# Performance work log

Hardware: AMD Instinct MI355X
Metric: run time of the kernel (lower is better)

The kernel has to match this reference:

```python
import jax, jax.numpy as jnp
import numpy as np

DT = 1.0       # integration timestep
THRESH = 0.5   # firing threshold (standard in this family of SNN repos)


def setup_inputs() -> dict:
    key = jax.random.key(0)
    ks = jax.random.split(key, 6)
    B, Din, Dout = 32768, 256, 512
    input_spike = jax.random.uniform(ks[0], (B, Din), dtype=jnp.float32)
    mem = jnp.zeros((B, Dout), jnp.float32)
    spike = jnp.zeros((B, Dout), jnp.float32)
    s_in = 1.0 / np.sqrt(Din)
    s_h = 1.0 / np.sqrt(Dout)
    W_dense = jax.random.uniform(ks[1], (Dout, Din), minval=-s_in, maxval=s_in, dtype=jnp.float32)
    b_dense = jax.random.uniform(ks[2], (Dout,), minval=-s_in, maxval=s_in, dtype=jnp.float32)
    W_rec = jax.random.uniform(ks[3], (Dout, Dout), minval=-s_h, maxval=s_h, dtype=jnp.float32)
    b_rec = jax.random.uniform(ks[4], (Dout,), minval=-s_h, maxval=s_h, dtype=jnp.float32)
    tau_m = 20.0 + 5.0 * jax.random.normal(ks[5], (Dout,), dtype=jnp.float32)
    return dict(input_spike=input_spike, mem=mem, spike=spike,
                W_dense=W_dense, b_dense=b_dense, W_rec=W_rec, b_rec=b_rec,
                tau_m=tau_m)


def reference(input_spike, mem, spike, W_dense, b_dense, W_rec, b_rec, tau_m):
    # d_input = dense(input_spike) + recurrent(spike)
    d_input = (jnp.einsum('bi,oi->bo', input_spike, W_dense) + b_dense
               + jnp.einsum('bh,oh->bo', spike, W_rec) + b_rec)
    # LIF neuron dynamics: exponential membrane decay, soft reset, heaviside spike
    alpha = jnp.exp(-DT / tau_m)                                   # [Dout]
    mem_new = mem * alpha + (1.0 - alpha) * d_input - THRESH * spike
    spike_new = (mem_new - THRESH > 0).astype(mem_new.dtype)
    return mem_new, spike_new
```

## Files before the change

### kernel.cpp

```cpp
#include <hip/hip_runtime.h>
#include <math.h>

typedef short  short8  __attribute__((ext_vector_type(8)));
typedef short  short4v __attribute__((ext_vector_type(4)));
typedef float  f32x4   __attribute__((ext_vector_type(4)));

#define BATCH 32768
#define DIN   256
#define DOUT  512
#define BM    128
#define BN    64

#define WS_FLAGS 0
#define WS_WD2   4096
#define WS_WR2   (4096 + 262144)
#define WS_X2    (266240 + 524288)

__device__ __forceinline__ short f2bf(float v) {
    unsigned u = __float_as_uint(v);
    u += 0x7fffu + ((u >> 16) & 1u);
    return (short)(u >> 16);
}

__global__ __launch_bounds__(1024) void spike_flag_kernel(
    const float* __restrict__ SPK, int* __restrict__ flags)
{
    __shared__ int s_any;
    if (threadIdx.x == 0) s_any = 0;
    __syncthreads();
    const f32x4* p = (const f32x4*)(SPK + (size_t)blockIdx.x * BM * DOUT);
    unsigned bits = 0;
#pragma unroll
    for (int i = 0; i < 16; i++) {
        f32x4 v = p[threadIdx.x + i * 1024];
        bits |= __float_as_uint(v[0]) | __float_as_uint(v[1])
              | __float_as_uint(v[2]) | __float_as_uint(v[3]);
    }
    if (bits) s_any = 1;
    __syncthreads();
    if (threadIdx.x == 0) flags[blockIdx.x] = s_any;
}

__global__ __launch_bounds__(256) void cvt_bf16_kernel(
    const float* __restrict__ src, short* __restrict__ dst, int n4)
{
    int i = blockIdx.x * 256 + threadIdx.x;
    if (i >= n4) return;
    f32x4 v = ((const f32x4*)src)[i];
    ((short4v*)dst)[i] = (short4v){f2bf(v[0]), f2bf(v[1]), f2bf(v[2]), f2bf(v[3])};
}

__global__ __launch_bounds__(256, 3) void spike_rnn_lif_kernel(
    const short* __restrict__ X2,
    const float* __restrict__ MEM,
    const float* __restrict__ SPK,
    const short* __restrict__ Wd2,
    const float* __restrict__ bd,
    const short* __restrict__ Wr2,
    const float* __restrict__ br,
    const float* __restrict__ tau,
    const int*   __restrict__ flags,
    float* __restrict__ out)
{
    __shared__ float sT[64 * 68];

    const int tid  = threadIdx.x;
    const int lane = tid & 63;
    const int w    = tid >> 6;
    const int wm   = w & 1;
    const int wn   = w >> 1;
    const int bn   = blockIdx.x;
    const int bm   = blockIdx.y;
    const int m0   = bm * BM;
    const int n0   = bn * BN;
    const int col  = lane & 15;
    const int quad = lane >> 4;

    const bool has_spk = (flags[bm] != 0);

    const int c4   = tid & 15;
    const int ncol = n0 + c4 * 4;
    f32x4 mv0[4];
#pragma unroll
    for (int it = 0; it < 4; it++) {
        int row = m0 + ((tid + it * 256) >> 4);
        mv0[it] = __builtin_nontemporal_load(
                      (const f32x4*)(MEM + (size_t)row * DOUT + ncol));
    }

    f32x4 acc[4][2];
#pragma unroll
    for (int i = 0; i < 4; i++)
#pragma unroll
        for (int j = 0; j < 2; j++)
            acc[i][j] = (f32x4){0.f, 0.f, 0.f, 0.f};

    {
        const short* Abase = X2  + (size_t)(m0 + wm * 64 + col) * DIN + quad * 8;
        const short* Bbase = Wd2 + (size_t)(n0 + wn * 32 + col) * DIN + quad * 8;

#define LOAD_AB(kk, aa, bb)                                                   \
        do {                                                                  \
            int k_ = (kk) * 32;                                               \
            _Pragma("unroll")                                                 \
            for (int t = 0; t < 4; t++)                                       \
                aa[t] = *(const short8*)(Abase + (size_t)t * 16 * DIN + k_);  \
            _Pragma("unroll")                                                 \
            for (int t = 0; t < 2; t++)                                       \
                bb[t] = *(const short8*)(Bbase + (size_t)t * 16 * DIN + k_);  \
        } while (0)

#define MFMA_AB(aa, bb)                                                       \
        do {                                                                  \
            _Pragma("unroll")                                                 \
            for (int i = 0; i < 4; i++)                                       \
                _Pragma("unroll")                                             \
                for (int j = 0; j < 2; j++)                                   \
                    acc[i][j] = __builtin_amdgcn_mfma_f32_16x16x32_bf16(      \
                        aa[i], bb[j], acc[i][j], 0, 0, 0);                    \
        } while (0)

        short8 a0[4], b0[2], a1[4], b1[2];
        LOAD_AB(0, a0, b0);
#pragma unroll
        for (int kp = 0; kp < 4; kp++) {
            LOAD_AB(2 * kp + 1, a1, b1);
            MFMA_AB(a0, b0);
            if (kp < 3) LOAD_AB(2 * kp + 2, a0, b0);
            MFMA_AB(a1, b1);
        }
#undef LOAD_AB
    }

    if (has_spk) {
        const float* Abase = SPK + (size_t)(m0 + wm * 64 + col) * DOUT + quad * 8;
        const short* Bbase = Wr2 + (size_t)(n0 + wn * 32 + col) * DOUT + quad * 8;
#pragma unroll 4
        for (int ks = 0; ks < 16; ks++) {
            int k = ks * 32;
            short8 a[4], b[2];
#pragma unroll
            for (int t = 0; t < 4; t++) {
                const float* ap = Abase + (size_t)t * 16 * DOUT + k;
                f32x4 lo = *(const f32x4*)ap;
                f32x4 hi = *(const f32x4*)(ap + 4);
                a[t] = (short8){f2bf(lo[0]), f2bf(lo[1]), f2bf(lo[2]), f2bf(lo[3]),
                                f2bf(hi[0]), f2bf(hi[1]), f2bf(hi[2]), f2bf(hi[3])};
            }
#pragma unroll
            for (int t = 0; t < 2; t++)
                b[t] = *(const short8*)(Bbase + (size_t)t * 16 * DOUT + k);
            MFMA_AB(a, b);
        }
    }
#undef MFMA_AB

    f32x4 mv1[4];
#pragma unroll
    for (int it = 0; it < 4; it++) {
        int row = m0 + 64 + ((tid + it * 256) >> 4);
        mv1[it] = __builtin_nontemporal_load(
                      (const f32x4*)(MEM + (size_t)row * DOUT + ncol));
    }

    float al[4], oma[4], bs[4];
#pragma unroll
    for (int q = 0; q < 4; q++) {
        al[q]  = expf(-1.0f / tau[ncol + q]);
        oma[q] = 1.0f - al[q];
        bs[q]  = bd[ncol + q] + br[ncol + q];
    }

#pragma unroll
    for (int c = 0; c < 2; c++) {
        if (c) __syncthreads();
        if (wm == c) {
#pragma unroll
            for (int j = 0; j < 2; j++)
#pragma unroll
                for (int i = 0; i < 4; i++)
#pragma unroll
                    for (int rr = 0; rr < 4; rr++)
                        sT[(i * 16 + quad * 4 + rr) * 68 + wn * 32 + j * 16 + col]
                            = acc[i][j][rr];
        }
        __syncthreads();
#pragma unroll
        for (int it = 0; it < 4; it++) {
            int p   = tid + it * 256;
            int r2  = p >> 4;
            int row = m0 + c * 64 + r2;
            f32x4 d  = *(const f32x4*)(sT + r2 * 68 + c4 * 4);
            f32x4 mv = c ? mv1[it] : mv0[it];
            f32x4 sv = has_spk ? *(const f32x4*)(SPK + (size_t)row * DOUT + ncol)
                               : (f32x4){0.f, 0.f, 0.f, 0.f};
            f32x4 mn, sp;
#pragma unroll
            for (int q = 0; q < 4; q++) {
                mn[q] = mv[q] * al[q] + oma[q] * (d[q] + bs[q]) - 0.5f * sv[q];
                sp[q] = (mn[q] - 0.5f > 0.0f) ? 1.0f : 0.0f;
            }
            __builtin_nontemporal_store(mn,
                (f32x4*)(out + (size_t)row * DOUT + ncol));
            __builtin_nontemporal_store(sp,
                (f32x4*)(out + (size_t)BATCH * DOUT + (size_t)row * DOUT + ncol));
        }
    }
}

extern "C" void kernel_launch(void* const* d_in, const int* in_sizes, int n_in,
                              void* d_out, int out_size, void* d_ws, size_t ws_size,
                              hipStream_t stream) {
    const float* X   = (const float*)d_in[0];
    const float* MEM = (const float*)d_in[1];
    const float* SPK = (const float*)d_in[2];
    const float* Wd  = (const float*)d_in[3];
    const float* bd  = (const float*)d_in[4];
    const float* Wr  = (const float*)d_in[5];
    const float* br  = (const float*)d_in[6];
    const float* tau = (const float*)d_in[7];

    char*  ws    = (char*)d_ws;
    int*   flags = (int*)  (ws + WS_FLAGS);
    short* Wd2   = (short*)(ws + WS_WD2);
    short* Wr2   = (short*)(ws + WS_WR2);
    short* X2    = (short*)(ws + WS_X2);

    spike_flag_kernel<<<BATCH / BM, 1024, 0, stream>>>(SPK, flags);
    {
        int n4 = DOUT * DIN / 4;
        cvt_bf16_kernel<<<(n4 + 255) / 256, 256, 0, stream>>>(Wd, Wd2, n4);
    }
    {
        int n4 = DOUT * DOUT / 4;
        cvt_bf16_kernel<<<(n4 + 255) / 256, 256, 0, stream>>>(Wr, Wr2, n4);
    }
    {
        int n4 = BATCH * DIN / 4;
        cvt_bf16_kernel<<<(n4 + 255) / 256, 256, 0, stream>>>(X, X2, n4);
    }

    dim3 grid(DOUT / BN, BATCH / BM);
    spike_rnn_lif_kernel<<<grid, 256, 0, stream>>>(X2, MEM, SPK, Wd2, bd, Wr2, br,
                                                   tau, flags, (float*)d_out);
}
```

Measured before the change: 311.4 us.

## Fuse prepass kernels, swizzle GEMM block order, hoist second MEM load

Merges the spike-flag scan and the three bf16 conversion kernels into one 2048-block prepass that sets per-row-tile flags with atomicOr after a memset, cutting launch count. The main kernel becomes a 1D grid remapped so that groups of 8 row tiles share column blocks, aiming for better L2 reuse of weights and activations. The second half of the MEM tile is now loaded at kernel start alongside the first, so its latency hides behind the GEMM, at the cost of extra live registers.

```diff
diff --git a/kernel.cpp b/kernel.cpp
--- a/kernel.cpp
+++ b/kernel.cpp
@@ -22,32 +22,52 @@
     return (short)(u >> 16);
 }
 
-__global__ __launch_bounds__(1024) void spike_flag_kernel(
-    const float* __restrict__ SPK, int* __restrict__ flags)
+__global__ __launch_bounds__(256) void prepass_kernel(
+    const float* __restrict__ SPK, const float* __restrict__ X,
+    const float* __restrict__ Wd,  const float* __restrict__ Wr,
+    int* __restrict__ flags, short* __restrict__ X2,
+    short* __restrict__ Wd2, short* __restrict__ Wr2)
 {
-    __shared__ int s_any;
-    if (threadIdx.x == 0) s_any = 0;
-    __syncthreads();
-    const f32x4* p = (const f32x4*)(SPK + (size_t)blockIdx.x * BM * DOUT);
-    unsigned bits = 0;
-#pragma unroll
-    for (int i = 0; i < 16; i++) {
-        f32x4 v = p[threadIdx.x + i * 1024];
-        bits |= __float_as_uint(v[0]) | __float_as_uint(v[1])
-              | __float_as_uint(v[2]) | __float_as_uint(v[3]);
-    }
-    if (bits) s_any = 1;
-    __syncthreads();
-    if (threadIdx.x == 0) flags[blockIdx.x] = s_any;
-}
-
-__global__ __launch_bounds__(256) void cvt_bf16_kernel(
-    const float* __restrict__ src, short* __restrict__ dst, int n4)
-{
-    int i = blockIdx.x * 256 + threadIdx.x;
-    if (i >= n4) return;
-    f32x4 v = ((const f32x4*)src)[i];
-    ((short4v*)dst)[i] = (short4v){f2bf(v[0]), f2bf(v[1]), f2bf(v[2]), f2bf(v[3])};
+    const int b   = blockIdx.x;
+    const int tid = threadIdx.x;
+
+    {
+        unsigned bits = 0;
+        const f32x4* p = (const f32x4*)SPK + (size_t)b * 2048;
+#pragma unroll
+        for (int j = 0; j < 8; j++) {
+            f32x4 v = p[tid + j * 256];
+            bits |= __float_as_uint(v[0]) | __float_as_uint(v[1])
+                  | __float_as_uint(v[2]) | __float_as_uint(v[3]);
+        }
+        if (__any(bits != 0) && (tid & 63) == 0)
+            atomicOr(&flags[b >> 3], 1);
+    }
+
+    {
+        const f32x4* src = (const f32x4*)X + (size_t)b * 1024;
+        short4v*     dst = (short4v*)X2   + (size_t)b * 1024;
+#pragma unroll
+        for (int j = 0; j < 4; j++) {
+            f32x4 v = src[tid + j * 256];
+            dst[tid + j * 256] = (short4v){f2bf(v[0]), f2bf(v[1]),
+                                           f2bf(v[2]), f2bf(v[3])};
+        }
+    }
+
+    {
+        int idx = b * 256 + tid;
+        if (idx < 32768) {
+            f32x4 v = ((const f32x4*)Wd)[idx];
+            ((short4v*)Wd2)[idx] = (short4v){f2bf(v[0]), f2bf(v[1]),
+                                             f2bf(v[2]), f2bf(v[3])};
+        } else if (idx < 98304) {
+            int k = idx - 32768;
+            f32x4 v = ((const f32x4*)Wr)[k];
+            ((short4v*)Wr2)[k] = (short4v){f2bf(v[0]), f2bf(v[1]),
+                                           f2bf(v[2]), f2bf(v[3])};
+        }
+    }
 }
 
 __global__ __launch_bounds__(256, 3) void spike_rnn_lif_kernel(
@@ -69,8 +89,10 @@
     const int w    = tid >> 6;
     const int wm   = w & 1;
     const int wn   = w >> 1;
-    const int bn   = blockIdx.x;
-    const int bm   = blockIdx.y;
+
+    const int L    = blockIdx.x;
+    const int bm   = ((L >> 6) << 3) + (L & 7);
+    const int bn   = (L >> 3) & 7;
     const int m0   = bm * BM;
     const int n0   = bn * BN;
     const int col  = lane & 15;
@@ -80,12 +102,14 @@
 
     const int c4   = tid & 15;
     const int ncol = n0 + c4 * 4;
-    f32x4 mv0[4];
+    f32x4 mv0[4], mv1[4];
 #pragma unroll
     for (int it = 0; it < 4; it++) {
-        int row = m0 + ((tid + it * 256) >> 4);
+        int r2 = (tid + it * 256) >> 4;
         mv0[it] = __builtin_nontemporal_load(
-                      (const f32x4*)(MEM + (size_t)row * DOUT + ncol));
+                      (const f32x4*)(MEM + (size_t)(m0 + r2) * DOUT + ncol));
+        mv1[it] = __builtin_nontemporal_load(
+                      (const f32x4*)(MEM + (size_t)(m0 + 64 + r2) * DOUT + ncol));
     }
 
     f32x4 acc[4][2];
@@ -154,14 +178,6 @@
         }
     }
 #undef MFMA_AB
-
-    f32x4 mv1[4];
-#pragma unroll
-    for (int it = 0; it < 4; it++) {
-        int row = m0 + 64 + ((tid + it * 256) >> 4);
-        mv1[it] = __builtin_nontemporal_load(
-                      (const f32x4*)(MEM + (size_t)row * DOUT + ncol));
-    }
 
     float al[4], oma[4], bs[4];
 #pragma unroll
@@ -226,21 +242,9 @@
     short* Wr2   = (short*)(ws + WS_WR2);
     short* X2    = (short*)(ws + WS_X2);
 
-    spike_flag_kernel<<<BATCH / BM, 1024, 0, stream>>>(SPK, flags);
-    {
-        int n4 = DOUT * DIN / 4;
-        cvt_bf16_kernel<<<(n4 + 255) / 256, 256, 0, stream>>>(Wd, Wd2, n4);
-    }
-    {
-        int n4 = DOUT * DOUT / 4;
-        cvt_bf16_kernel<<<(n4 + 255) / 256, 256, 0, stream>>>(Wr, Wr2, n4);
-    }
-    {
-        int n4 = BATCH * DIN / 4;
-        cvt_bf16_kernel<<<(n4 + 255) / 256, 256, 0, stream>>>(X, X2, n4);
-    }
-
-    dim3 grid(DOUT / BN, BATCH / BM);
-    spike_rnn_lif_kernel<<<grid, 256, 0, stream>>>(X2, MEM, SPK, Wd2, bd, Wr2, br,
+    hipMemsetAsync(flags, 0, 256 * sizeof(int), stream);
+    prepass_kernel<<<2048, 256, 0, stream>>>(SPK, X, Wd, Wr, flags, X2, Wd2, Wr2);
+
+    spike_rnn_lif_kernel<<<2048, 256, 0, stream>>>(X2, MEM, SPK, Wd2, bd, Wr2, br,
                                                    tau, flags, (float*)d_out);
 }
```

New measurement: 304.6 us. 1.02x faster.
